# Kernel tuning notes

Measured on AMD Instinct MI355X. Metric: run time of the kernel, lower is better.

Reference implementation:

```python
import jax, jax.numpy as jnp
import numpy as np

D_MODEL = 1024
NUM_HEADS = 16
D_K = D_MODEL // NUM_HEADS


def setup_inputs() -> dict:
    key = jax.random.key(0)
    ks = jax.random.split(key, 12)
    B, L, D = 1, 4096, D_MODEL
    s = 1.0 / np.sqrt(D)
    return {
        "q": jax.random.normal(ks[0], (B, L, D), jnp.float32),
        "k": jax.random.normal(ks[1], (B, L, D), jnp.float32),
        "v": jax.random.normal(ks[2], (B, L, D), jnp.float32),
        "wq": jax.random.normal(ks[3], (D, D), jnp.float32) * s,
        "bq": jnp.zeros((D,), jnp.float32),
        "wk": jax.random.normal(ks[4], (D, D), jnp.float32) * s,
        "bk": jnp.zeros((D,), jnp.float32),
        "wv": jax.random.normal(ks[5], (D, D), jnp.float32) * s,
        "bv": jnp.zeros((D,), jnp.float32),
        "wo": jax.random.normal(ks[6], (D, D), jnp.float32) * s,
        "bo": jnp.zeros((D,), jnp.float32),
    }


def reference(q, k, v, wq, bq, wk, bk, wv, bv, wo, bo):
    B, L, D = q.shape
    H, dk = NUM_HEADS, D_K
    # linear projections then split heads: [B, L, D] -> [B, H, L, dk]
    def proj(x, w, b):
        return (x @ w.T + b).reshape(B, L, H, dk).transpose(0, 2, 1, 3)
    qh = proj(q, wq, bq)
    kh = proj(k, wk, bk)
    vh = proj(v, wv, bv)
    scores = jnp.einsum("bhqd,bhkd->bhqk", qh, kh) / jnp.sqrt(jnp.float32(dk))
    attn = jax.nn.softmax(scores, axis=-1)  # [B, H, L, L]
    out = jnp.einsum("bhqk,bhkd->bhqd", attn, vh)
    out = out.transpose(0, 2, 1, 3).reshape(B, L, D)
    return out @ wo.T + bo
```

## Files before the change

### kernel.cpp

```cpp
#include <hip/hip_runtime.h>
#include <hip/hip_bf16.h>
#include <stdint.h>


typedef __bf16 bf16_t;
typedef __bf16 bf16x8 __attribute__((ext_vector_type(8)));
typedef __bf16 bf16x4 __attribute__((ext_vector_type(4)));
typedef float f32x4 __attribute__((ext_vector_type(4)));
typedef unsigned short u16x8 __attribute__((ext_vector_type(8)));

#define MFMA_BF16 __builtin_amdgcn_mfma_f32_16x16x32_bf16

__device__ __forceinline__ void async_copy16(const void* g, void* lds) {
  __builtin_amdgcn_global_load_lds(
      (__attribute__((address_space(1))) void*)(uintptr_t)g,
      (__attribute__((address_space(3))) void*)lds, 16, 0, 0);
}

__global__ __launch_bounds__(256) void cast_f32_bf16(
    const float* __restrict__ s0, bf16_t* __restrict__ d0, int n0,
    const float* __restrict__ s1, bf16_t* __restrict__ d1, int n1,
    const float* __restrict__ s2, bf16_t* __restrict__ d2, int n2,
    const float* __restrict__ s3, bf16_t* __restrict__ d3, int n3,
    const float* __restrict__ s4, bf16_t* __restrict__ d4, int n4,
    const float* __restrict__ s5, bf16_t* __restrict__ d5, int n5,
    const float* __restrict__ s6, bf16_t* __restrict__ d6, int n6) {
  const float* s;
  bf16_t* d;
  int n;
  switch (blockIdx.z) {
    case 0: s = s0; d = d0; n = n0; break;
    case 1: s = s1; d = d1; n = n1; break;
    case 2: s = s2; d = d2; n = n2; break;
    case 3: s = s3; d = d3; n = n3; break;
    case 4: s = s4; d = d4; n = n4; break;
    case 5: s = s5; d = d5; n = n5; break;
    default: s = s6; d = d6; n = n6; break;
  }
  const int i = (blockIdx.x * 256 + threadIdx.x) * 8;
  if (i >= n) return;
  float4 a = *(const float4*)(s + i);
  float4 b = *(const float4*)(s + i + 4);
  bf16x8 o;
  o[0] = (bf16_t)a.x; o[1] = (bf16_t)a.y; o[2] = (bf16_t)a.z; o[3] = (bf16_t)a.w;
  o[4] = (bf16_t)b.x; o[5] = (bf16_t)b.y; o[6] = (bf16_t)b.z; o[7] = (bf16_t)b.w;
  *(bf16x8*)(d + i) = o;
}

template <typename CT>
__global__ __launch_bounds__(256) void gemm3_bt(
    const bf16_t* __restrict__ A0, const bf16_t* __restrict__ W0,
    const float* __restrict__ b0, CT* __restrict__ C0,
    const bf16_t* __restrict__ A1, const bf16_t* __restrict__ W1,
    const float* __restrict__ b1, CT* __restrict__ C1,
    const bf16_t* __restrict__ A2, const bf16_t* __restrict__ W2,
    const float* __restrict__ b2, CT* __restrict__ C2,
    int M, int N, int K) {
  const bf16_t *A, *W;
  const float* bias;
  CT* C;
  if (blockIdx.z == 0)      { A = A0; W = W0; bias = b0; C = C0; }
  else if (blockIdx.z == 1) { A = A1; W = W1; bias = b1; C = C1; }
  else                      { A = A2; W = W2; bias = b2; C = C2; }

  __shared__ bf16_t As[128][32];
  __shared__ bf16_t Bs[128][32];

  const int t = threadIdx.x;
  const int w = t >> 6, lane = t & 63;
  const int quad = lane >> 4, l16 = lane & 15;
  const int wr = w >> 1, wc = w & 1;
  const int m0 = blockIdx.x * 128;
  const int n0 = blockIdx.y * 128;
  const int srow = lane >> 2;
  const int scol = (lane & 3) * 8;

  f32x4 acc[4][4] = {};

  for (int k0 = 0; k0 < K; k0 += 32) {
    async_copy16(&A[(size_t)(m0 + (2 * w) * 16 + srow) * K + k0 + scol],
                 (char*)As + (2 * w) * 1024);
    async_copy16(&A[(size_t)(m0 + (2 * w + 1) * 16 + srow) * K + k0 + scol],
                 (char*)As + (2 * w + 1) * 1024);
    async_copy16(&W[(size_t)(n0 + (2 * w) * 16 + srow) * K + k0 + scol],
                 (char*)Bs + (2 * w) * 1024);
    async_copy16(&W[(size_t)(n0 + (2 * w + 1) * 16 + srow) * K + k0 + scol],
                 (char*)Bs + (2 * w + 1) * 1024);
    __syncthreads();

    bf16x8 af[4], bfr[4];
#pragma unroll
    for (int mt = 0; mt < 4; mt++)
      af[mt] = *(const bf16x8*)&As[wr * 64 + mt * 16 + l16][quad * 8];
#pragma unroll
    for (int nt = 0; nt < 4; nt++)
      bfr[nt] = *(const bf16x8*)&Bs[wc * 64 + nt * 16 + l16][quad * 8];
#pragma unroll
    for (int mt = 0; mt < 4; mt++)
#pragma unroll
      for (int nt = 0; nt < 4; nt++)
        acc[mt][nt] = MFMA_BF16(af[mt], bfr[nt], acc[mt][nt], 0, 0, 0);
    __syncthreads();
  }

#pragma unroll
  for (int nt = 0; nt < 4; nt++) {
    const int col = n0 + wc * 64 + nt * 16 + l16;
    const float bb = bias[col];
#pragma unroll
    for (int mt = 0; mt < 4; mt++) {
#pragma unroll
      for (int r = 0; r < 4; r++) {
        const int row = m0 + wr * 64 + mt * 16 + quad * 4 + r;
        C[(size_t)row * N + col] = (CT)(acc[mt][nt][r] + bb);
      }
    }
  }
}

__global__ __launch_bounds__(256) void frag_tile(
    const bf16_t* __restrict__ s0, bf16_t* __restrict__ d0,
    const bf16_t* __restrict__ s1, bf16_t* __restrict__ d1,
    const bf16_t* __restrict__ s2, bf16_t* __restrict__ d2) {
  const bf16_t* src;
  bf16_t* dst;
  const int z = blockIdx.z;
  if (z == 0)      { src = s0; dst = d0; }
  else if (z == 1) { src = s1; dst = d1; }
  else             { src = s2; dst = d2; }

  const int h = blockIdx.y;
  const int l0 = blockIdx.x * 64;
  const int t = threadIdx.x;

  __shared__ ushort Ts[64][72];

#pragma unroll
  for (int p = 0; p < 2; p++) {
    const int r = p * 32 + (t >> 3);
    const int c = (t & 7) * 8;
    float4 v = *(const float4*)(src + (size_t)(l0 + r) * 1024 + h * 64 + c);
    *(float4*)&Ts[r][c] = v;
  }
  __syncthreads();

  if (z < 2) {
    const float qscale = 0.125f * 1.44269504088896340736f;
#pragma unroll
    for (int p = 0; p < 2; p++) {
      const int gi = p * 256 + t;
      const int l16 = gi & 15, quad = (gi >> 4) & 3, kc = (gi >> 6) & 1;
      const int tl = gi >> 7;
      float4 v = *(const float4*)&Ts[tl * 16 + l16][kc * 32 + quad * 8];
      if (z == 0) {
        bf16x8 b = *(bf16x8*)&v;
#pragma unroll
        for (int e = 0; e < 8; e++) b[e] = (bf16_t)((float)b[e] * qscale);
        v = *(float4*)&b;
      }
      *(float4*)(dst + (size_t)(h * 256 + (l0 >> 4) + tl) * 1024 +
                 (size_t)(kc * 64 + quad * 16 + l16) * 8) = v;
    }
  } else {
#pragma unroll
    for (int p = 0; p < 2; p++) {
      const int gi = p * 256 + t;
      const int l16 = gi & 15, quad = (gi >> 4) & 3, kvc = (gi >> 6) & 1;
      const int dkt = gi >> 7;
      u16x8 tmp;
#pragma unroll
      for (int e = 0; e < 8; e++)
        tmp[e] = Ts[kvc * 32 + quad * 8 + e][dkt * 16 + l16];
      *(u16x8*)(dst + (size_t)(h * 256 + (l0 >> 6) * 4 + dkt) * 1024 +
                (size_t)(kvc * 64 + quad * 16 + l16) * 8) = tmp;
    }
  }
}

__global__ __launch_bounds__(256, 2) void flash_attn(
    const bf16_t* __restrict__ Qt, const bf16_t* __restrict__ Kt,
    const bf16_t* __restrict__ Vt, bf16_t* __restrict__ O, int L) {
  const int h = blockIdx.y;
  const int t = threadIdx.x;
  const int w = t >> 6, lane = t & 63;
  const int quad = lane >> 4, l16 = lane & 15;
  const int tq0 = blockIdx.x * 8 + w * 2;

  __shared__ bf16_t Kst[2][4096];
  __shared__ bf16_t Vst[2][4096];
  __shared__ bf16_t Pb[4][32][72];

  const size_t hb = (size_t)h * 256 * 1024;

  bf16x8 qa[2][2];
#pragma unroll
  for (int qt = 0; qt < 2; qt++)
#pragma unroll
    for (int kc = 0; kc < 2; kc++)
      qa[qt][kc] = *(const bf16x8*)(Qt + hb + (size_t)(tq0 + qt) * 1024 +
                                    kc * 512 + lane * 8);

#define STAGE(it_, buf_)                                                     \
  {                                                                          \
    const size_t cb = hb + (size_t)(it_) * 4096;                             \
    async_copy16(Kt + cb + (size_t)t * 8, (char*)&Kst[buf_][0] + w * 1024);  \
    async_copy16(Kt + cb + (size_t)(256 + t) * 8,                            \
                 (char*)&Kst[buf_][0] + 4096 + w * 1024);                    \
    async_copy16(Vt + cb + (size_t)t * 8, (char*)&Vst[buf_][0] + w * 1024);  \
    async_copy16(Vt + cb + (size_t)(256 + t) * 8,                            \
                 (char*)&Vst[buf_][0] + 4096 + w * 1024);                    \
  }

  STAGE(0, 0);

  f32x4 oT[2][4] = {};
  float ls[2] = {0.f, 0.f};

  const int NIT = L / 64;
  for (int it = 0; it < NIT; it++) {
    const int buf = it & 1;
    __syncthreads();
    if (it + 1 < NIT) STAGE(it + 1, buf ^ 1);

    bf16x8 kb[4][2], vb[4][2];
#pragma unroll
    for (int tt = 0; tt < 4; tt++)
#pragma unroll
      for (int kc = 0; kc < 2; kc++)
        kb[tt][kc] = *(const bf16x8*)((const char*)&Kst[buf][0] + tt * 2048 +
                                      kc * 1024 + lane * 16);
#pragma unroll
    for (int dkt = 0; dkt < 4; dkt++)
#pragma unroll
      for (int kvc = 0; kvc < 2; kvc++)
        vb[dkt][kvc] = *(const bf16x8*)((const char*)&Vst[buf][0] +
                                        dkt * 2048 + kvc * 1024 + lane * 16);

#pragma unroll
    for (int qt = 0; qt < 2; qt++) {
      f32x4 sT[4];
#pragma unroll
      for (int tt = 0; tt < 4; tt++) {
        f32x4 z = {0.f, 0.f, 0.f, 0.f};
        z = MFMA_BF16(kb[tt][0], qa[qt][0], z, 0, 0, 0);
        z = MFMA_BF16(kb[tt][1], qa[qt][1], z, 0, 0, 0);
        sT[tt] = z;
      }
#pragma unroll
      for (int tt = 0; tt < 4; tt++) {
        bf16x4 pk;
        float rs = 0.f;
#pragma unroll
        for (int r = 0; r < 4; r++) {
          const float p = __builtin_amdgcn_exp2f(sT[tt][r]);
          rs += p;
          pk[r] = (bf16_t)p;
        }
        ls[qt] += rs;
        *(bf16x4*)&Pb[w][qt * 16 + l16][tt * 16 + quad * 4] = pk;
      }
    }

#pragma unroll
    for (int qt = 0; qt < 2; qt++) {
      const bf16x8 pf0 = *(const bf16x8*)&Pb[w][qt * 16 + l16][quad * 8];
      const bf16x8 pf1 = *(const bf16x8*)&Pb[w][qt * 16 + l16][32 + quad * 8];
#pragma unroll
      for (int dkt = 0; dkt < 4; dkt++) {
        oT[qt][dkt] = MFMA_BF16(vb[dkt][0], pf0, oT[qt][dkt], 0, 0, 0);
        oT[qt][dkt] = MFMA_BF16(vb[dkt][1], pf1, oT[qt][dkt], 0, 0, 0);
      }
    }
  }
#undef STAGE

#pragma unroll
  for (int qt = 0; qt < 2; qt++) {
    float l = ls[qt];
    l += __shfl_xor(l, 16);
    l += __shfl_xor(l, 32);
    const float inv = 1.0f / l;
    const size_t row = (size_t)(tq0 + qt) * 16 + l16;
#pragma unroll
    for (int dkt = 0; dkt < 4; dkt++)
#pragma unroll
      for (int r = 0; r < 4; r++)
        O[row * 1024 + h * 64 + dkt * 16 + quad * 4 + r] =
            (bf16_t)(oT[qt][dkt][r] * inv);
  }
}

extern "C" void kernel_launch(void* const* d_in, const int* in_sizes, int n_in,
                              void* d_out, int out_size, void* d_ws,
                              size_t ws_size, hipStream_t stream) {
  const float* q  = (const float*)d_in[0];
  const float* k  = (const float*)d_in[1];
  const float* v  = (const float*)d_in[2];
  const float* wq = (const float*)d_in[3];
  const float* bq = (const float*)d_in[4];
  const float* wk = (const float*)d_in[5];
  const float* bk = (const float*)d_in[6];
  const float* wv = (const float*)d_in[7];
  const float* bv = (const float*)d_in[8];
  const float* wo = (const float*)d_in[9];
  const float* bo = (const float*)d_in[10];
  float* out = (float*)d_out;

  const int L = 4096, D = 1024;
  const int nLD = L * D;
  const int nDD = D * D;
  bf16_t* p = (bf16_t*)d_ws;
  bf16_t* qb  = p; p += nLD;
  bf16_t* kb  = p; p += nLD;
  bf16_t* vb  = p; p += nLD;
  bf16_t* wqb = p; p += nDD;
  bf16_t* wkb = p; p += nDD;
  bf16_t* wvb = p; p += nDD;
  bf16_t* wob = p; p += nDD;
  bf16_t* Qp  = p; p += nLD;
  bf16_t* Kp  = p; p += nLD;
  bf16_t* Vp  = p; p += nLD;
  bf16_t* Qt  = p; p += nLD;
  bf16_t* Kt  = p; p += nLD;
  bf16_t* Vt  = p; p += nLD;
  bf16_t* Op  = Qp;

  dim3 blk(256);
  cast_f32_bf16<<<dim3(nLD / (256 * 8), 1, 7), blk, 0, stream>>>(
      q, qb, nLD, k, kb, nLD, v, vb, nLD, wq, wqb, nDD, wk, wkb, nDD,
      wv, wvb, nDD, wo, wob, nDD);
  gemm3_bt<bf16_t><<<dim3(L / 128, D / 128, 3), blk, 0, stream>>>(
      qb, wqb, bq, Qp, kb, wkb, bk, Kp, vb, wvb, bv, Vp, L, D, D);
  frag_tile<<<dim3(L / 64, 16, 3), blk, 0, stream>>>(Qp, Qt, Kp, Kt, Vp, Vt);
  flash_attn<<<dim3(L / 128, 16), blk, 0, stream>>>(Qt, Kt, Vt, Op, L);
  gemm3_bt<float><<<dim3(L / 128, D / 128, 1), blk, 0, stream>>>(
      Op, wob, bo, out, Op, wob, bo, out, Op, wob, bo, out, L, D, D);
}
```

Measured before the change: 272.2 us.

## Fuse fragment-layout permutation into QKV GEMM epilogue and read V directly

The QKV projection GEMM now writes its outputs straight into the MFMA-fragment tiled layouts that flash attention consumes, with the Q scale folded in. This removes the separate frag_tile kernel and its intermediate buffers. Flash attention also stops staging V through LDS and loads V fragments directly from global memory each iteration, which frees LDS but puts global-load latency on the critical path. The epilogue scatter writes are narrow (2-byte or 8-byte) stores and may coalesce poorly.

```diff
diff --git a/kernel.cpp b/kernel.cpp
--- a/kernel.cpp
+++ b/kernel.cpp
@@ -7,7 +7,6 @@
 typedef __bf16 bf16x8 __attribute__((ext_vector_type(8)));
 typedef __bf16 bf16x4 __attribute__((ext_vector_type(4)));
 typedef float f32x4 __attribute__((ext_vector_type(4)));
-typedef unsigned short u16x8 __attribute__((ext_vector_type(8)));
 
 #define MFMA_BF16 __builtin_amdgcn_mfma_f32_16x16x32_bf16
 
@@ -47,21 +46,22 @@
   *(bf16x8*)(d + i) = o;
 }
 
-template <typename CT>
-__global__ __launch_bounds__(256) void gemm3_bt(
+__global__ __launch_bounds__(256) void gemm_qkv(
     const bf16_t* __restrict__ A0, const bf16_t* __restrict__ W0,
-    const float* __restrict__ b0, CT* __restrict__ C0,
+    const float* __restrict__ b0,
     const bf16_t* __restrict__ A1, const bf16_t* __restrict__ W1,
-    const float* __restrict__ b1, CT* __restrict__ C1,
+    const float* __restrict__ b1,
     const bf16_t* __restrict__ A2, const bf16_t* __restrict__ W2,
-    const float* __restrict__ b2, CT* __restrict__ C2,
-    int M, int N, int K) {
+    const float* __restrict__ b2,
+    bf16_t* __restrict__ Qt, bf16_t* __restrict__ Kt,
+    bf16_t* __restrict__ Vt, int M, int N, int K) {
   const bf16_t *A, *W;
   const float* bias;
-  CT* C;
-  if (blockIdx.z == 0)      { A = A0; W = W0; bias = b0; C = C0; }
-  else if (blockIdx.z == 1) { A = A1; W = W1; bias = b1; C = C1; }
-  else                      { A = A2; W = W2; bias = b2; C = C2; }
+  bf16_t* C;
+  const int z = blockIdx.z;
+  if (z == 0)      { A = A0; W = W0; bias = b0; C = Qt; }
+  else if (z == 1) { A = A1; W = W1; bias = b1; C = Kt; }
+  else             { A = A2; W = W2; bias = b2; C = Vt; }
 
   __shared__ bf16_t As[128][32];
   __shared__ bf16_t Bs[128][32];
@@ -103,6 +103,91 @@
     __syncthreads();
   }
 
+  if (z < 2) {
+    const float scale = (z == 0) ? 0.125f * 1.44269504088896340736f : 1.0f;
+#pragma unroll
+    for (int nt = 0; nt < 4; nt++) {
+      const int col = n0 + wc * 64 + nt * 16 + l16;
+      const float bb = bias[col];
+      const size_t base_nt = (size_t)(col >> 6) * 262144 +
+                             ((col >> 5) & 1) * 512 + ((col >> 3) & 3) * 128 +
+                             (col & 7);
+#pragma unroll
+      for (int mt = 0; mt < 4; mt++) {
+        const int tile = (m0 >> 4) + wr * 4 + mt;
+        const size_t tb = base_nt + (size_t)tile * 1024;
+#pragma unroll
+        for (int r = 0; r < 4; r++)
+          C[tb + (quad * 4 + r) * 8] = (bf16_t)((acc[mt][nt][r] + bb) * scale);
+      }
+    }
+  } else {
+#pragma unroll
+    for (int nt = 0; nt < 4; nt++) {
+      const int col = n0 + wc * 64 + nt * 16 + l16;
+      const int dk = col & 63;
+      const float bb = bias[col];
+      const size_t hb = (size_t)(col >> 6) * 262144 +
+                        (size_t)(dk >> 4) * 1024 + (dk & 15) * 8;
+#pragma unroll
+      for (int mt = 0; mt < 4; mt++) {
+        const int rb = m0 + wr * 64 + mt * 16 + quad * 4;
+        const size_t addr = hb + (size_t)(rb >> 6) * 4096 +
+                            ((rb >> 5) & 1) * 512 + ((rb >> 3) & 3) * 128 +
+                            (rb & 7);
+        bf16x4 pk;
+#pragma unroll
+        for (int r = 0; r < 4; r++) pk[r] = (bf16_t)(acc[mt][nt][r] + bb);
+        *(bf16x4*)&C[addr] = pk;
+      }
+    }
+  }
+}
+
+__global__ __launch_bounds__(256) void gemm_out(
+    const bf16_t* __restrict__ A, const bf16_t* __restrict__ W,
+    const float* __restrict__ bias, float* __restrict__ C, int M, int N,
+    int K) {
+  __shared__ bf16_t As[128][32];
+  __shared__ bf16_t Bs[128][32];
+
+  const int t = threadIdx.x;
+  const int w = t >> 6, lane = t & 63;
+  const int quad = lane >> 4, l16 = lane & 15;
+  const int wr = w >> 1, wc = w & 1;
+  const int m0 = blockIdx.x * 128;
+  const int n0 = blockIdx.y * 128;
+  const int srow = lane >> 2;
+  const int scol = (lane & 3) * 8;
+
+  f32x4 acc[4][4] = {};
+
+  for (int k0 = 0; k0 < K; k0 += 32) {
+    async_copy16(&A[(size_t)(m0 + (2 * w) * 16 + srow) * K + k0 + scol],
+                 (char*)As + (2 * w) * 1024);
+    async_copy16(&A[(size_t)(m0 + (2 * w + 1) * 16 + srow) * K + k0 + scol],
+                 (char*)As + (2 * w + 1) * 1024);
+    async_copy16(&W[(size_t)(n0 + (2 * w) * 16 + srow) * K + k0 + scol],
+                 (char*)Bs + (2 * w) * 1024);
+    async_copy16(&W[(size_t)(n0 + (2 * w + 1) * 16 + srow) * K + k0 + scol],
+                 (char*)Bs + (2 * w + 1) * 1024);
+    __syncthreads();
+
+    bf16x8 af[4], bfr[4];
+#pragma unroll
+    for (int mt = 0; mt < 4; mt++)
+      af[mt] = *(const bf16x8*)&As[wr * 64 + mt * 16 + l16][quad * 8];
+#pragma unroll
+    for (int nt = 0; nt < 4; nt++)
+      bfr[nt] = *(const bf16x8*)&Bs[wc * 64 + nt * 16 + l16][quad * 8];
+#pragma unroll
+    for (int mt = 0; mt < 4; mt++)
+#pragma unroll
+      for (int nt = 0; nt < 4; nt++)
+        acc[mt][nt] = MFMA_BF16(af[mt], bfr[nt], acc[mt][nt], 0, 0, 0);
+    __syncthreads();
+  }
+
 #pragma unroll
   for (int nt = 0; nt < 4; nt++) {
     const int col = n0 + wc * 64 + nt * 16 + l16;
@@ -112,67 +197,8 @@
 #pragma unroll
       for (int r = 0; r < 4; r++) {
         const int row = m0 + wr * 64 + mt * 16 + quad * 4 + r;
-        C[(size_t)row * N + col] = (CT)(acc[mt][nt][r] + bb);
-      }
-    }
-  }
-}
-
-__global__ __launch_bounds__(256) void frag_tile(
-    const bf16_t* __restrict__ s0, bf16_t* __restrict__ d0,
-    const bf16_t* __restrict__ s1, bf16_t* __restrict__ d1,
-    const bf16_t* __restrict__ s2, bf16_t* __restrict__ d2) {
-  const bf16_t* src;
-  bf16_t* dst;
-  const int z = blockIdx.z;
-  if (z == 0)      { src = s0; dst = d0; }
-  else if (z == 1) { src = s1; dst = d1; }
-  else             { src = s2; dst = d2; }
-
-  const int h = blockIdx.y;
-  const int l0 = blockIdx.x * 64;
-  const int t = threadIdx.x;
-
-  __shared__ ushort Ts[64][72];
-
-#pragma unroll
-  for (int p = 0; p < 2; p++) {
-    const int r = p * 32 + (t >> 3);
-    const int c = (t & 7) * 8;
-    float4 v = *(const float4*)(src + (size_t)(l0 + r) * 1024 + h * 64 + c);
-    *(float4*)&Ts[r][c] = v;
-  }
-  __syncthreads();
-
-  if (z < 2) {
-    const float qscale = 0.125f * 1.44269504088896340736f;
-#pragma unroll
-    for (int p = 0; p < 2; p++) {
-      const int gi = p * 256 + t;
-      const int l16 = gi & 15, quad = (gi >> 4) & 3, kc = (gi >> 6) & 1;
-      const int tl = gi >> 7;
-      float4 v = *(const float4*)&Ts[tl * 16 + l16][kc * 32 + quad * 8];
-      if (z == 0) {
-        bf16x8 b = *(bf16x8*)&v;
-#pragma unroll
-        for (int e = 0; e < 8; e++) b[e] = (bf16_t)((float)b[e] * qscale);
-        v = *(float4*)&b;
-      }
-      *(float4*)(dst + (size_t)(h * 256 + (l0 >> 4) + tl) * 1024 +
-                 (size_t)(kc * 64 + quad * 16 + l16) * 8) = v;
-    }
-  } else {
-#pragma unroll
-    for (int p = 0; p < 2; p++) {
-      const int gi = p * 256 + t;
-      const int l16 = gi & 15, quad = (gi >> 4) & 3, kvc = (gi >> 6) & 1;
-      const int dkt = gi >> 7;
-      u16x8 tmp;
-#pragma unroll
-      for (int e = 0; e < 8; e++)
-        tmp[e] = Ts[kvc * 32 + quad * 8 + e][dkt * 16 + l16];
-      *(u16x8*)(dst + (size_t)(h * 256 + (l0 >> 6) * 4 + dkt) * 1024 +
-                (size_t)(kvc * 64 + quad * 16 + l16) * 8) = tmp;
+        C[(size_t)row * N + col] = acc[mt][nt][r] + bb;
+      }
     }
   }
 }
@@ -187,10 +213,9 @@
   const int tq0 = blockIdx.x * 8 + w * 2;
 
   __shared__ bf16_t Kst[2][4096];
-  __shared__ bf16_t Vst[2][4096];
   __shared__ bf16_t Pb[4][32][72];
 
-  const size_t hb = (size_t)h * 256 * 1024;
+  const size_t hb = (size_t)h * 262144;
 
   bf16x8 qa[2][2];
 #pragma unroll
@@ -206,9 +231,6 @@
     async_copy16(Kt + cb + (size_t)t * 8, (char*)&Kst[buf_][0] + w * 1024);  \
     async_copy16(Kt + cb + (size_t)(256 + t) * 8,                            \
                  (char*)&Kst[buf_][0] + 4096 + w * 1024);                    \
-    async_copy16(Vt + cb + (size_t)t * 8, (char*)&Vst[buf_][0] + w * 1024);  \
-    async_copy16(Vt + cb + (size_t)(256 + t) * 8,                            \
-                 (char*)&Vst[buf_][0] + 4096 + w * 1024);                    \
   }
 
   STAGE(0, 0);
@@ -222,19 +244,21 @@
     __syncthreads();
     if (it + 1 < NIT) STAGE(it + 1, buf ^ 1);
 
-    bf16x8 kb[4][2], vb[4][2];
+    bf16x8 vb[4][2];
+#pragma unroll
+    for (int dkt = 0; dkt < 4; dkt++)
+#pragma unroll
+      for (int kvc = 0; kvc < 2; kvc++)
+        vb[dkt][kvc] = *(const bf16x8*)(Vt + hb + (size_t)(it * 4 + dkt) * 1024 +
+                                        kvc * 512 + lane * 8);
+
+    bf16x8 kb[4][2];
 #pragma unroll
     for (int tt = 0; tt < 4; tt++)
 #pragma unroll
       for (int kc = 0; kc < 2; kc++)
         kb[tt][kc] = *(const bf16x8*)((const char*)&Kst[buf][0] + tt * 2048 +
                                       kc * 1024 + lane * 16);
-#pragma unroll
-    for (int dkt = 0; dkt < 4; dkt++)
-#pragma unroll
-      for (int kvc = 0; kvc < 2; kvc++)
-        vb[dkt][kvc] = *(const bf16x8*)((const char*)&Vst[buf][0] +
-                                        dkt * 2048 + kvc * 1024 + lane * 16);
 
 #pragma unroll
     for (int qt = 0; qt < 2; qt++) {
@@ -317,22 +341,18 @@
   bf16_t* wkb = p; p += nDD;
   bf16_t* wvb = p; p += nDD;
   bf16_t* wob = p; p += nDD;
-  bf16_t* Qp  = p; p += nLD;
-  bf16_t* Kp  = p; p += nLD;
-  bf16_t* Vp  = p; p += nLD;
   bf16_t* Qt  = p; p += nLD;
   bf16_t* Kt  = p; p += nLD;
   bf16_t* Vt  = p; p += nLD;
-  bf16_t* Op  = Qp;
+  bf16_t* Op  = qb;
 
   dim3 blk(256);
   cast_f32_bf16<<<dim3(nLD / (256 * 8), 1, 7), blk, 0, stream>>>(
       q, qb, nLD, k, kb, nLD, v, vb, nLD, wq, wqb, nDD, wk, wkb, nDD,
       wv, wvb, nDD, wo, wob, nDD);
-  gemm3_bt<bf16_t><<<dim3(L / 128, D / 128, 3), blk, 0, stream>>>(
-      qb, wqb, bq, Qp, kb, wkb, bk, Kp, vb, wvb, bv, Vp, L, D, D);
-  frag_tile<<<dim3(L / 64, 16, 3), blk, 0, stream>>>(Qp, Qt, Kp, Kt, Vp, Vt);
+  gemm_qkv<<<dim3(L / 128, D / 128, 3), blk, 0, stream>>>(
+      qb, wqb, bq, kb, wkb, bk, vb, wvb, bv, Qt, Kt, Vt, L, D, D);
   flash_attn<<<dim3(L / 128, 16), blk, 0, stream>>>(Qt, Kt, Vt, Op, L);
-  gemm3_bt<float><<<dim3(L / 128, D / 128, 1), blk, 0, stream>>>(
-      Op, wob, bo, out, Op, wob, bo, out, Op, wob, bo, out, L, D, D);
-}
+  gemm_out<<<dim3(L / 128, D / 128), blk, 0, stream>>>(Op, wob, bo, out, L, D,
+                                                       D);
+}
```

Measured after the change: 275.3 us. About the same (+1.1%).
